# Performance work log

Hardware: AMD Instinct MI355X
Metric: run time of the kernel (lower is better)

The kernel has to match this reference:

```python
import jax, jax.numpy as jnp
import numpy as np

DIM = 1024
NUM_HEADS = 32
HEAD_DIM = 32
T = 2048
SCALE = 0.12
ROT_BASE = HEAD_DIM * 4  # Rotary(head_dim, max_seq_len, head_dim*4)
RMS_EPS = 1.1920929e-07  # torch float32 finfo eps (F.rms_norm default)


def _rms_norm(x):
    ms = jnp.mean(jnp.square(x), axis=-1, keepdims=True)
    return x * jax.lax.rsqrt(ms + RMS_EPS)


def _rotary_tables(seq_len):
    # modded-nanogpt half-truncated rotary: frequencies on first quarter, zeros on second
    quarter = HEAD_DIM // 4
    af = (1.0 / ROT_BASE) ** jnp.linspace(0.0, 1.0, quarter, dtype=jnp.float32)
    af = jnp.concatenate([af, jnp.zeros(quarter, dtype=jnp.float32)])  # [hd/2]
    theta = jnp.arange(seq_len, dtype=jnp.float32)[:, None] * af[None, :]  # [T, hd/2]
    return jnp.cos(theta), jnp.sin(theta)


def _apply_rotary(x, cos, sin):
    # x: [B, T, H, hd]; cos/sin: [T, hd/2]
    x1, x2 = jnp.split(x, 2, axis=-1)
    c = cos[None, :, None, :]
    s = sin[None, :, None, :]
    y1 = x1 * c + x2 * s
    y2 = -x1 * s + x2 * c
    return jnp.concatenate([y1, y2], axis=-1)


def setup_inputs() -> dict:
    key = jax.random.key(0)
    k1, k2, k3, k4 = jax.random.split(key, 4)
    std = 0.5 * DIM ** (-0.5)
    bound = (3.0 ** 0.5) * std
    x = jax.random.normal(k1, (1, T, DIM), dtype=jnp.float32)
    ve = jax.random.normal(k2, (1, T, NUM_HEADS * HEAD_DIM), dtype=jnp.float32)
    qkv_w = jax.random.uniform(k3, (3, NUM_HEADS * HEAD_DIM, DIM), dtype=jnp.float32,
                               minval=-bound, maxval=bound)
    lambdas = jnp.array([0.5, 0.5], dtype=jnp.float32)
    # original zero-inits c_proj; use small random so output/grads are nontrivial
    c_proj_w = jax.random.normal(k4, (DIM, NUM_HEADS * HEAD_DIM), dtype=jnp.float32) * 0.02
    return {"x": x, "ve": ve, "qkv_w": qkv_w, "lambdas": lambdas, "c_proj_w": c_proj_w}


def reference(x, ve, qkv_w, lambdas, c_proj_w):
    B, T_, D = x.shape
    H, hd = NUM_HEADS, HEAD_DIM
    # fused QKV projection: F.linear(x, qkv_w.flatten(end_dim=1))
    w = qkv_w.reshape(3 * H * hd, D)
    qkv = jnp.einsum('btd,ed->bte', x, w).reshape(B, T_, 3 * H, hd)
    q, k, v = jnp.split(qkv, 3, axis=2)  # each [B, T, H, hd]
    q = _rms_norm(q)
    k = _rms_norm(k)
    cos, sin = _rotary_tables(T_)
    q = _apply_rotary(q, cos, sin)
    k = _apply_rotary(k, cos, sin)
    v = lambdas[0] * v + lambdas[1] * ve.reshape(B, T_, H, hd)
    # causal attention with fixed scale 0.12
    scores = jnp.einsum('bqhd,bkhd->bhqk', q, k) * SCALE
    causal = jnp.tril(jnp.ones((T_, T_), dtype=bool))
    scores = jnp.where(causal[None, None, :, :], scores, -jnp.inf)
    attn = jax.nn.softmax(scores, axis=-1)
    y = jnp.einsum('bhqk,bkhd->bqhd', attn, v).reshape(B, T_, H * hd)
    return jnp.einsum('bte,de->btd', y, c_proj_w)
```

## Files before the change

kernel.cpp:

```cpp
#include <hip/hip_runtime.h>
#include <hip/hip_bf16.h>

#define NHEADS 32
#define HD_ 32
#define TSEQ 2048
#define SCALE_ 0.12f
#define LOG2E_ 1.44269504088896f
#define RMS_EPS_ 1.1920929e-07f

typedef unsigned short ushort_t;
typedef __bf16 bf16_t;
typedef __attribute__((ext_vector_type(8))) bf16_t bf16x8;
typedef __attribute__((ext_vector_type(4))) float f32x4;
typedef __attribute__((ext_vector_type(8))) unsigned short u16x8;

__device__ __forceinline__ ushort_t f2bfn(float f){
    __hip_bfloat16 b = __float2bfloat16(f);
    return *reinterpret_cast<ushort_t*>(&b);
}
__device__ __forceinline__ float bf2f(ushort_t s){
    union { unsigned u; float f; } v; v.u = ((unsigned)s) << 16;
    return v.f;
}
__device__ __forceinline__ float fexp2(float x){
#if __has_builtin(__builtin_amdgcn_exp2f)
    return __builtin_amdgcn_exp2f(x);
#else
    return exp2f(x);
#endif
}
__device__ __forceinline__ void gld16(const void* g, void* l){
    __builtin_amdgcn_global_load_lds(
        (const __attribute__((address_space(1))) unsigned int*)g,
        (__attribute__((address_space(3))) unsigned int*)l,
        16, 0, 0);
}

__global__ __launch_bounds__(256) void k_prep(const float* __restrict__ x,
                                              const float* __restrict__ qkw,
                                              const float* __restrict__ cpw,
                                              ushort_t* __restrict__ xb,
                                              ushort_t* __restrict__ wb,
                                              ushort_t* __restrict__ cpb,
                                              float* __restrict__ cost,
                                              float* __restrict__ sint)
{
    const int n1 = TSEQ * 1024 / 4, n2 = 3 * 1024 * 1024 / 4, n3 = 1024 * 1024 / 4;
    int i = blockIdx.x * 256 + threadIdx.x;
    if (i < n1 + n2 + n3){
        const float* src; ushort_t* dst; int j = i;
        if (j < n1){ src = x; dst = xb; }
        else if (j < n1 + n2){ j -= n1; src = qkw; dst = wb; }
        else { j -= n1 + n2; src = cpw; dst = cpb; }
        float4 v = ((const float4*)src)[j];
        ushort4 o;
        o.x = f2bfn(v.x); o.y = f2bfn(v.y); o.z = f2bfn(v.z); o.w = f2bfn(v.w);
        ((ushort4*)dst)[j] = o;
    } else {
        int g = i - (n1 + n2 + n3);
        if (g < TSEQ * 16){
            int t = g >> 4, ii = g & 15;
            float c = 1.0f, s = 0.0f;
            if (ii < 8){
                float af = powf(1.0f / 128.0f, (float)ii * (1.0f / 7.0f));
                sincosf((float)t * af, &s, &c);
            }
            cost[g] = c; sint[g] = s;
        }
    }
}

__global__ __launch_bounds__(256, 3) void k_gemm_qkv(const ushort_t* __restrict__ A,
                                                     const ushort_t* __restrict__ B,
                                                     const float* __restrict__ ve,
                                                     const float* __restrict__ lam,
                                                     const float* __restrict__ cost,
                                                     const float* __restrict__ sint,
                                                     ushort_t* __restrict__ qb,
                                                     ushort_t* __restrict__ kbuf,
                                                     ushort_t* __restrict__ vtb)
{
    const int K = 1024;
    __shared__ __align__(16) ushort_t As[2][128 * 32];
    __shared__ __align__(16) ushort_t Bs[2][64 * 32];
    const int tid = threadIdx.x;
    const int lane = tid & 63;
    const int w = tid >> 6;
    const int wr = w >> 1, wc = w & 1;
    const int l15 = lane & 15, hi = lane >> 4;
    const int m0 = blockIdx.y * 128, n0 = blockIdx.x * 64;
    const int sec = n0 >> 10;
    const int h = ((n0 & 1023) >> 5) + wc;
    const int srow = lane >> 2, scol = (lane & 3) * 8;

    f32x4 acc[4][2] = {};

    auto stage = [&](int k0, int buf){
        #pragma unroll
        for (int i = 0; i < 2; ++i){
            int c = w + i * 4;
            gld16(&A[(size_t)(m0 + c * 16 + srow) * K + k0 + scol], &As[buf][c * 512]);
        }
        gld16(&B[(size_t)(n0 + w * 16 + srow) * K + k0 + scol], &Bs[buf][w * 512]);
    };

    stage(0, 0);
    int cur = 0;
    for (int k0 = 0; k0 < K; k0 += 32){
        __syncthreads();
        if (k0 + 32 < K) stage(k0 + 32, cur ^ 1);
        bf16x8 af[4], bfr[2];
        #pragma unroll
        for (int mi = 0; mi < 4; ++mi)
            af[mi] = *(const bf16x8*)&As[cur][(wr * 64 + mi * 16 + l15) * 32 + hi * 8];
        #pragma unroll
        for (int ni = 0; ni < 2; ++ni)
            bfr[ni] = *(const bf16x8*)&Bs[cur][(wc * 32 + ni * 16 + l15) * 32 + hi * 8];
        #pragma unroll
        for (int mi = 0; mi < 4; ++mi)
            #pragma unroll
            for (int ni = 0; ni < 2; ++ni)
                acc[mi][ni] = __builtin_amdgcn_mfma_f32_16x16x32_bf16(af[mi], bfr[ni], acc[mi][ni], 0, 0, 0);
        cur ^= 1;
    }

    if (sec < 2){
        ushort_t* dst = (sec == 0) ? qb : kbuf;
        const float qscl = (sec == 0) ? SCALE_ * LOG2E_ : 1.0f;
        #pragma unroll
        for (int mi = 0; mi < 4; ++mi){
            #pragma unroll
            for (int r = 0; r < 4; ++r){
                const int t = m0 + wr * 64 + mi * 16 + hi * 4 + r;
                float v0 = acc[mi][0][r], v1 = acc[mi][1][r];
                float ss = v0 * v0 + v1 * v1;
                ss += __shfl_xor(ss, 1);
                ss += __shfl_xor(ss, 2);
                ss += __shfl_xor(ss, 4);
                ss += __shfl_xor(ss, 8);
                const float inv = rsqrtf(ss * (1.0f / 32.0f) + RMS_EPS_);
                const float c = cost[t * 16 + l15], s = sint[t * 16 + l15];
                const float n0v = v0 * inv, n1v = v1 * inv;
                const float o0 = (n0v * c + n1v * s) * qscl;
                const float o1 = (n1v * c - n0v * s) * qscl;
                size_t base = ((size_t)h * TSEQ + t) * 32;
                dst[base + l15]      = f2bfn(o0);
                dst[base + 16 + l15] = f2bfn(o1);
            }
        }
    } else {
        const float l0 = lam[0], l1 = lam[1];
        __syncthreads();
        ushort_t* vt = &As[0][0] + w * 2048;
        #pragma unroll
        for (int ni = 0; ni < 2; ++ni){
            const int d = ni * 16 + l15;
            #pragma unroll
            for (int mi = 0; mi < 4; ++mi){
                #pragma unroll
                for (int r = 0; r < 4; ++r){
                    const int t = m0 + wr * 64 + mi * 16 + hi * 4 + r;
                    const int tl = mi * 16 + hi * 4 + r;
                    float vef = ve[(size_t)t * 1024 + h * 32 + d];
                    float ov = l0 * acc[mi][ni][r] + l1 * vef;
                    const int g = (tl >> 3) ^ (d & 7);
                    vt[d * 64 + g * 8 + (tl & 7)] = f2bfn(ov);
                }
            }
        }
        __syncthreads();
        const int tc = lane & 7;
        #pragma unroll
        for (int p = 0; p < 4; ++p){
            const int d = p * 8 + (lane >> 3);
            const int g = tc ^ (d & 7);
            u16x8 o = *(const u16x8*)&vt[d * 64 + g * 8];
            *(u16x8*)&vtb[((size_t)h * HD_ + d) * TSEQ + m0 + wr * 64 + tc * 8] = o;
        }
    }
}

__global__ __launch_bounds__(256) void k_gemm_out(const ushort_t* __restrict__ A,
                                                  const ushort_t* __restrict__ B,
                                                  float* __restrict__ C,
                                                  int M, int N, int K)
{
    __shared__ __align__(16) ushort_t As[2][64 * 64];
    __shared__ __align__(16) ushort_t Bs[2][64 * 64];
    const int tid = threadIdx.x;
    const int lane = tid & 63;
    const int w = tid >> 6;
    const int wr = w >> 1, wc = w & 1;
    const int l15 = lane & 15, hi = lane >> 4;
    const int m0 = blockIdx.y * 64, n0 = blockIdx.x * 64;
    const int srow = lane >> 3, scol = (lane & 7) * 8;

    f32x4 acc[2][2] = {};

    auto stage = [&](int k0, int buf){
        #pragma unroll
        for (int i = 0; i < 2; ++i){
            int c = w * 2 + i;
            gld16(&A[(size_t)(m0 + c * 8 + srow) * K + k0 + scol], &As[buf][c * 512]);
            gld16(&B[(size_t)(n0 + c * 8 + srow) * K + k0 + scol], &Bs[buf][c * 512]);
        }
    };

    stage(0, 0);
    int cur = 0;
    for (int k0 = 0; k0 < K; k0 += 64){
        __syncthreads();
        if (k0 + 64 < K) stage(k0 + 64, cur ^ 1);
        bf16x8 af[2][2], bfr[2][2];
        #pragma unroll
        for (int mi = 0; mi < 2; ++mi)
            #pragma unroll
            for (int sub = 0; sub < 2; ++sub)
                af[mi][sub] = *(const bf16x8*)&As[cur][(wr * 32 + mi * 16 + l15) * 64 + sub * 32 + hi * 8];
        #pragma unroll
        for (int ni = 0; ni < 2; ++ni)
            #pragma unroll
            for (int sub = 0; sub < 2; ++sub)
                bfr[ni][sub] = *(const bf16x8*)&Bs[cur][(wc * 32 + ni * 16 + l15) * 64 + sub * 32 + hi * 8];
        #pragma unroll
        for (int sub = 0; sub < 2; ++sub)
            #pragma unroll
            for (int mi = 0; mi < 2; ++mi)
                #pragma unroll
                for (int ni = 0; ni < 2; ++ni)
                    acc[mi][ni] = __builtin_amdgcn_mfma_f32_16x16x32_bf16(af[mi][sub], bfr[ni][sub], acc[mi][ni], 0, 0, 0);
        cur ^= 1;
    }

    #pragma unroll
    for (int mi = 0; mi < 2; ++mi)
        #pragma unroll
        for (int ni = 0; ni < 2; ++ni)
            #pragma unroll
            for (int r = 0; r < 4; ++r){
                int row = m0 + wr * 32 + mi * 16 + hi * 4 + r;
                int col = n0 + wc * 32 + ni * 16 + l15;
                C[(size_t)row * N + col] = acc[mi][ni][r];
            }
}

template<bool MASK>
__device__ __forceinline__ void chain_step(const bf16x8* kf, const bf16x8* vv0, const bf16x8* vv1,
                                           ushort_t* pb, const bf16x8& qf,
                                           int kb0, int qrow, int l15, int hi,
                                           f32x4& a0, f32x4& a1, float& lp)
{
    f32x4 s[4];
    __builtin_amdgcn_s_setprio(1);
    #pragma unroll
    for (int ni = 0; ni < 4; ++ni){
        f32x4 z = {0.f, 0.f, 0.f, 0.f};
        s[ni] = __builtin_amdgcn_mfma_f32_16x16x32_bf16(kf[ni], qf, z, 0, 0, 0);
    }
    __builtin_amdgcn_s_setprio(0);
    if (MASK){
        const int relc = qrow - kb0 - 4 * hi;
        #pragma unroll
        for (int ni = 0; ni < 4; ++ni)
            #pragma unroll
            for (int r = 0; r < 4; ++r)
                if (16 * ni + r > relc) s[ni][r] = -1e30f;
    }
    float ps = 0.f;
    #pragma unroll
    for (int ni = 0; ni < 4; ++ni)
        #pragma unroll
        for (int r = 0; r < 4; ++r){
            float p = fexp2(s[ni][r]);
            s[ni][r] = p;
            ps += p;
        }
    lp += ps;
    #pragma unroll
    for (int ni = 0; ni < 4; ++ni){
        ushort4 pk;
        pk.x = f2bfn(s[ni][0]); pk.y = f2bfn(s[ni][1]);
        pk.z = f2bfn(s[ni][2]); pk.w = f2bfn(s[ni][3]);
        *(ushort4*)&pb[l15 * 72 + ni * 16 + hi * 4] = pk;
    }
    __builtin_amdgcn_s_setprio(1);
    #pragma unroll
    for (int kk = 0; kk < 2; ++kk){
        bf16x8 pf = *(const bf16x8*)&pb[l15 * 72 + kk * 32 + hi * 8];
        a0 = __builtin_amdgcn_mfma_f32_16x16x32_bf16(vv0[kk], pf, a0, 0, 0, 0);
        a1 = __builtin_amdgcn_mfma_f32_16x16x32_bf16(vv1[kk], pf, a1, 0, 0, 0);
    }
    __builtin_amdgcn_s_setprio(0);
}

__global__ __launch_bounds__(256, 4) void k_attn(const ushort_t* __restrict__ qb,
                                                 const ushort_t* __restrict__ kb,
                                                 const ushort_t* __restrict__ vtb,
                                                 ushort_t* __restrict__ yb)
{
    const int bid = blockIdx.x;
    const int xcd = bid & 7, idx = bid >> 3;
    const int h  = xcd * 4 + (idx & 3);
    const int qt = 31 - (idx >> 2);
    const int tid = threadIdx.x;
    const int w = tid >> 6, lane = tid & 63;
    const int l15 = lane & 15, hi = lane >> 4;

    __shared__ __align__(16) ushort_t Kbuf[2][64 * 32];
    __shared__ __align__(16) ushort_t Vbuf[2][32 * 64];
    __shared__ __align__(16) ushort_t Pbuf[4][16 * 72];

    const ushort_t* kb_h = kb + (size_t)h * TSEQ * HD_;
    const ushort_t* vt_h = vtb + (size_t)h * HD_ * TSEQ;
    const ushort_t* qb_h = qb + (size_t)h * TSEQ * HD_;

    const int qw = qt * 64 + w * 16;
    const bf16x8 qf = *(const bf16x8*)&qb_h[(size_t)(qw + l15) * 32 + hi * 8];

    const int krow = w * 16 + (lane >> 2);
    const int kcol = (lane & 3) * 8;
    const int vrow = w * 8 + (lane >> 3);
    const int vslot = (lane & 7) ^ (vrow & 7);
    auto stage = [&](int kt, int buf){
        const int kb0 = kt * 64;
        gld16(&kb_h[(size_t)(kb0 + krow) * 32 + kcol], &Kbuf[buf][w * 512]);
        gld16(&vt_h[(size_t)vrow * TSEQ + kb0 + vslot * 8], &Vbuf[buf][w * 512]);
    };

    f32x4 a0 = {0.f,0.f,0.f,0.f}, a1 = a0;
    float lp = 0.f;
    ushort_t* pb = &Pbuf[w][0];

    const int nT = qt + 1;
    stage(0, 0);
    int cur = 0;
    for (int kt = 0; kt < nT; ++kt){
        __syncthreads();
        if (kt + 1 < nT) stage(kt + 1, cur ^ 1);
        const int kb0 = kt * 64;
        bf16x8 kf[4], vv0[2], vv1[2];
        #pragma unroll
        for (int ni = 0; ni < 4; ++ni)
            kf[ni] = *(const bf16x8*)&Kbuf[cur][(ni * 16 + l15) * 32 + hi * 8];
        #pragma unroll
        for (int kk = 0; kk < 2; ++kk){
            int sl = kk * 4 + hi;
            vv0[kk] = *(const bf16x8*)&Vbuf[cur][l15 * 64 + (sl ^ (l15 & 7)) * 8];
            vv1[kk] = *(const bf16x8*)&Vbuf[cur][(16 + l15) * 64 + (sl ^ (l15 & 7)) * 8];
        }
        if (kt < qt)
            chain_step<false>(kf, vv0, vv1, pb, qf, kb0, qw + l15, l15, hi, a0, a1, lp);
        else
            chain_step<true >(kf, vv0, vv1, pb, qf, kb0, qw + l15, l15, hi, a0, a1, lp);
        cur ^= 1;
    }

    lp += __shfl_xor(lp, 16);
    lp += __shfl_xor(lp, 32);
    float inv = 1.0f / lp;
    ushort4 o0, o1;
    o0.x = f2bfn(a0[0]*inv); o0.y = f2bfn(a0[1]*inv);
    o0.z = f2bfn(a0[2]*inv); o0.w = f2bfn(a0[3]*inv);
    o1.x = f2bfn(a1[0]*inv); o1.y = f2bfn(a1[1]*inv);
    o1.z = f2bfn(a1[2]*inv); o1.w = f2bfn(a1[3]*inv);
    size_t base = (size_t)(qw + l15) * 1024 + h * 32;
    *(ushort4*)&yb[base + hi * 4]      = o0;
    *(ushort4*)&yb[base + 16 + hi * 4] = o1;
}

extern "C" void kernel_launch(void* const* d_in, const int* in_sizes, int n_in,
                              void* d_out, int out_size, void* d_ws, size_t ws_size,
                              hipStream_t stream)
{
    const float* x   = (const float*)d_in[0];
    const float* ve  = (const float*)d_in[1];
    const float* qkw = (const float*)d_in[2];
    const float* lam = (const float*)d_in[3];
    const float* cpw = (const float*)d_in[4];

    char* ws = (char*)d_ws;
    size_t o = 0;
    auto take = [&](size_t bytes) -> char* {
        char* p = ws + o; o += (bytes + 255) & ~(size_t)255; return p;
    };
    ushort_t* xb   = (ushort_t*)take((size_t)TSEQ * 1024 * 2);
    ushort_t* wb   = (ushort_t*)take((size_t)3072 * 1024 * 2);
    ushort_t* cpb  = (ushort_t*)take((size_t)1024 * 1024 * 2);
    float*    cost = (float*)take((size_t)TSEQ * 16 * 4);
    float*    sint = (float*)take((size_t)TSEQ * 16 * 4);
    ushort_t* qb   = (ushort_t*)take((size_t)NHEADS * TSEQ * HD_ * 2);
    ushort_t* kb   = (ushort_t*)take((size_t)NHEADS * TSEQ * HD_ * 2 + 8192);
    ushort_t* vtb  = (ushort_t*)take((size_t)NHEADS * HD_ * TSEQ * 2 + 8192);
    ushort_t* yb   = xb;

    const int prep_items = (TSEQ * 1024 + 3 * 1024 * 1024 + 1024 * 1024) / 4 + TSEQ * 16;
    k_prep<<<(prep_items + 255) / 256, 256, 0, stream>>>(x, qkw, cpw, xb, wb, cpb, cost, sint);
    k_gemm_qkv<<<dim3(48, 16), 256, 0, stream>>>(xb, wb, ve, lam, cost, sint, qb, kb, vtb);
    k_attn<<<1024, 256, 0, stream>>>(qb, kb, vtb, yb);
    k_gemm_out<<<dim3(1024 / 64, TSEQ / 64), 256, 0, stream>>>(yb, cpb, (float*)d_out, TSEQ, 1024, 1024);
}
```

Measured before the change: 152.0 us.

## Fuse fp32-to-bf16 conversion and rotary tables into GEMMs, drop prep kernel

The separate prep kernel that cast x, qkv_w and c_proj_w to bf16 and precomputed cos/sin tables is removed. The QKV and output GEMMs now load fp32 tiles into registers, convert them to bf16 and write them to swizzled LDS, and rotary sin/cos is computed inline. Block indices are remapped with an XCD-aware grid. The attention K tile also gets an XOR swizzle against LDS bank conflicts. This saves one launch plus a full pass writing and rereading the bf16 copies. In exchange, the GEMMs read twice the global bytes per element and do conversion work on the critical path, because global_load_lds is replaced by register staging.

```diff
diff --git a/kernel.cpp b/kernel.cpp
--- a/kernel.cpp
+++ b/kernel.cpp
@@ -18,10 +18,6 @@
     __hip_bfloat16 b = __float2bfloat16(f);
     return *reinterpret_cast<ushort_t*>(&b);
 }
-__device__ __forceinline__ float bf2f(ushort_t s){
-    union { unsigned u; float f; } v; v.u = ((unsigned)s) << 16;
-    return v.f;
-}
 __device__ __forceinline__ float fexp2(float x){
 #if __has_builtin(__builtin_amdgcn_exp2f)
     return __builtin_amdgcn_exp2f(x);
@@ -35,47 +31,17 @@
         (__attribute__((address_space(3))) unsigned int*)l,
         16, 0, 0);
 }
-
-__global__ __launch_bounds__(256) void k_prep(const float* __restrict__ x,
-                                              const float* __restrict__ qkw,
-                                              const float* __restrict__ cpw,
-                                              ushort_t* __restrict__ xb,
-                                              ushort_t* __restrict__ wb,
-                                              ushort_t* __restrict__ cpb,
-                                              float* __restrict__ cost,
-                                              float* __restrict__ sint)
-{
-    const int n1 = TSEQ * 1024 / 4, n2 = 3 * 1024 * 1024 / 4, n3 = 1024 * 1024 / 4;
-    int i = blockIdx.x * 256 + threadIdx.x;
-    if (i < n1 + n2 + n3){
-        const float* src; ushort_t* dst; int j = i;
-        if (j < n1){ src = x; dst = xb; }
-        else if (j < n1 + n2){ j -= n1; src = qkw; dst = wb; }
-        else { j -= n1 + n2; src = cpw; dst = cpb; }
-        float4 v = ((const float4*)src)[j];
-        ushort4 o;
-        o.x = f2bfn(v.x); o.y = f2bfn(v.y); o.z = f2bfn(v.z); o.w = f2bfn(v.w);
-        ((ushort4*)dst)[j] = o;
-    } else {
-        int g = i - (n1 + n2 + n3);
-        if (g < TSEQ * 16){
-            int t = g >> 4, ii = g & 15;
-            float c = 1.0f, s = 0.0f;
-            if (ii < 8){
-                float af = powf(1.0f / 128.0f, (float)ii * (1.0f / 7.0f));
-                sincosf((float)t * af, &s, &c);
-            }
-            cost[g] = c; sint[g] = s;
-        }
-    }
-}
-
-__global__ __launch_bounds__(256, 3) void k_gemm_qkv(const ushort_t* __restrict__ A,
-                                                     const ushort_t* __restrict__ B,
+__device__ __forceinline__ u16x8 pack8(float4 a, float4 b){
+    u16x8 o;
+    o[0]=f2bfn(a.x); o[1]=f2bfn(a.y); o[2]=f2bfn(a.z); o[3]=f2bfn(a.w);
+    o[4]=f2bfn(b.x); o[5]=f2bfn(b.y); o[6]=f2bfn(b.z); o[7]=f2bfn(b.w);
+    return o;
+}
+
+__global__ __launch_bounds__(256, 3) void k_gemm_qkv(const float* __restrict__ X,
+                                                     const float* __restrict__ W,
                                                      const float* __restrict__ ve,
                                                      const float* __restrict__ lam,
-                                                     const float* __restrict__ cost,
-                                                     const float* __restrict__ sint,
                                                      ushort_t* __restrict__ qb,
                                                      ushort_t* __restrict__ kbuf,
                                                      ushort_t* __restrict__ vtb)
@@ -88,34 +54,50 @@
     const int w = tid >> 6;
     const int wr = w >> 1, wc = w & 1;
     const int l15 = lane & 15, hi = lane >> 4;
-    const int m0 = blockIdx.y * 128, n0 = blockIdx.x * 64;
-    const int sec = n0 >> 10;
-    const int h = ((n0 & 1023) >> 5) + wc;
-    const int srow = lane >> 2, scol = (lane & 3) * 8;
+
+    const int bid = blockIdx.x;
+    const int xcd = bid & 7, j = bid >> 3;
+    const int m0 = (xcd * 2 + (j & 1)) * 128;
+    const int nidx = j >> 1;
+    const int n0 = nidx * 64;
+    const int sec = nidx >> 4;
+    const int h = ((nidx & 15) << 1) + wc;
+
+    const int arow = tid >> 1, ahalf = tid & 1;
+    const int brow = tid >> 2, bq = tid & 3;
+    const int akey = (arow >> 1) & 3;
+    const int bkey = (brow >> 1) & 3;
+    float4 ra[4], rb[2];
+
+    auto loadRegs = [&](int k0){
+        const float4* pa = (const float4*)&X[(size_t)(m0 + arow) * K + k0 + ahalf * 16];
+        ra[0] = pa[0]; ra[1] = pa[1]; ra[2] = pa[2]; ra[3] = pa[3];
+        const float4* pb = (const float4*)&W[(size_t)(n0 + brow) * K + k0 + bq * 8];
+        rb[0] = pb[0]; rb[1] = pb[1];
+    };
+    auto writeLDS = [&](int buf){
+        *(u16x8*)&As[buf][arow * 32 + ((ahalf * 2 + 0) ^ akey) * 8] = pack8(ra[0], ra[1]);
+        *(u16x8*)&As[buf][arow * 32 + ((ahalf * 2 + 1) ^ akey) * 8] = pack8(ra[2], ra[3]);
+        *(u16x8*)&Bs[buf][brow * 32 + (bq ^ bkey) * 8] = pack8(rb[0], rb[1]);
+    };
 
     f32x4 acc[4][2] = {};
-
-    auto stage = [&](int k0, int buf){
-        #pragma unroll
-        for (int i = 0; i < 2; ++i){
-            int c = w + i * 4;
-            gld16(&A[(size_t)(m0 + c * 16 + srow) * K + k0 + scol], &As[buf][c * 512]);
-        }
-        gld16(&B[(size_t)(n0 + w * 16 + srow) * K + k0 + scol], &Bs[buf][w * 512]);
-    };
-
-    stage(0, 0);
+    const int kq = (l15 >> 1) & 3;
+    const int soff = (hi ^ kq) * 8;
+
+    loadRegs(0);
     int cur = 0;
     for (int k0 = 0; k0 < K; k0 += 32){
-        __syncthreads();
-        if (k0 + 32 < K) stage(k0 + 32, cur ^ 1);
+        writeLDS(cur);
+        __syncthreads();
+        if (k0 + 32 < K) loadRegs(k0 + 32);
         bf16x8 af[4], bfr[2];
         #pragma unroll
         for (int mi = 0; mi < 4; ++mi)
-            af[mi] = *(const bf16x8*)&As[cur][(wr * 64 + mi * 16 + l15) * 32 + hi * 8];
+            af[mi] = *(const bf16x8*)&As[cur][(wr * 64 + mi * 16 + l15) * 32 + soff];
         #pragma unroll
         for (int ni = 0; ni < 2; ++ni)
-            bfr[ni] = *(const bf16x8*)&Bs[cur][(wc * 32 + ni * 16 + l15) * 32 + hi * 8];
+            bfr[ni] = *(const bf16x8*)&Bs[cur][(wc * 32 + ni * 16 + l15) * 32 + soff];
         #pragma unroll
         for (int mi = 0; mi < 4; ++mi)
             #pragma unroll
@@ -127,6 +109,7 @@
     if (sec < 2){
         ushort_t* dst = (sec == 0) ? qb : kbuf;
         const float qscl = (sec == 0) ? SCALE_ * LOG2E_ : 1.0f;
+        const float fs = exp2f(-(float)l15);
         #pragma unroll
         for (int mi = 0; mi < 4; ++mi){
             #pragma unroll
@@ -139,7 +122,8 @@
                 ss += __shfl_xor(ss, 4);
                 ss += __shfl_xor(ss, 8);
                 const float inv = rsqrtf(ss * (1.0f / 32.0f) + RMS_EPS_);
-                const float c = cost[t * 16 + l15], s = sint[t * 16 + l15];
+                float c = 1.0f, s = 0.0f;
+                if (l15 < 8) sincosf((float)t * fs, &s, &c);
                 const float n0v = v0 * inv, n1v = v1 * inv;
                 const float o0 = (n0v * c + n1v * s) * qscl;
                 const float o1 = (n1v * c - n0v * s) * qscl;
@@ -180,48 +164,67 @@
     }
 }
 
-__global__ __launch_bounds__(256) void k_gemm_out(const ushort_t* __restrict__ A,
-                                                  const ushort_t* __restrict__ B,
-                                                  float* __restrict__ C,
-                                                  int M, int N, int K)
-{
-    __shared__ __align__(16) ushort_t As[2][64 * 64];
-    __shared__ __align__(16) ushort_t Bs[2][64 * 64];
+__global__ __launch_bounds__(256, 3) void k_gemm_out(const ushort_t* __restrict__ A,
+                                                     const float* __restrict__ W2,
+                                                     float* __restrict__ C)
+{
+    const int K = 1024, N = 1024;
+    __shared__ __align__(16) ushort_t As2[2][64 * 64];
+    __shared__ __align__(16) ushort_t Bs2[2][64 * 64];
     const int tid = threadIdx.x;
     const int lane = tid & 63;
     const int w = tid >> 6;
     const int wr = w >> 1, wc = w & 1;
     const int l15 = lane & 15, hi = lane >> 4;
-    const int m0 = blockIdx.y * 64, n0 = blockIdx.x * 64;
-    const int srow = lane >> 3, scol = (lane & 7) * 8;
-
-    f32x4 acc[2][2] = {};
-
-    auto stage = [&](int k0, int buf){
+
+    const int bid = blockIdx.x;
+    const int xcd = bid & 7, j = bid >> 3;
+    const int m0 = (xcd * 4 + (j & 3)) * 64;
+    const int n0 = (j >> 2) * 64;
+
+    const int srow = lane >> 3;
+    const int sslot = (lane & 7) ^ srow;
+    const int brow = tid >> 2, bq = tid & 3;
+    const int bkey = brow & 7;
+    float4 rb[4];
+
+    auto stageA = [&](int k0, int buf){
         #pragma unroll
         for (int i = 0; i < 2; ++i){
             int c = w * 2 + i;
-            gld16(&A[(size_t)(m0 + c * 8 + srow) * K + k0 + scol], &As[buf][c * 512]);
-            gld16(&B[(size_t)(n0 + c * 8 + srow) * K + k0 + scol], &Bs[buf][c * 512]);
-        }
-    };
-
-    stage(0, 0);
+            gld16(&A[(size_t)(m0 + c * 8 + srow) * K + k0 + sslot * 8], &As2[buf][c * 512]);
+        }
+    };
+    auto loadB = [&](int k0){
+        const float4* p = (const float4*)&W2[(size_t)(n0 + brow) * K + k0 + bq * 16];
+        rb[0] = p[0]; rb[1] = p[1]; rb[2] = p[2]; rb[3] = p[3];
+    };
+    auto writeB = [&](int buf){
+        *(u16x8*)&Bs2[buf][brow * 64 + ((bq * 2 + 0) ^ bkey) * 8] = pack8(rb[0], rb[1]);
+        *(u16x8*)&Bs2[buf][brow * 64 + ((bq * 2 + 1) ^ bkey) * 8] = pack8(rb[2], rb[3]);
+    };
+
+    f32x4 acc[2][2] = {};
+    const int rkey = l15 & 7;
+
+    loadB(0);
+    stageA(0, 0);
     int cur = 0;
     for (int k0 = 0; k0 < K; k0 += 64){
-        __syncthreads();
-        if (k0 + 64 < K) stage(k0 + 64, cur ^ 1);
+        writeB(cur);
+        __syncthreads();
+        if (k0 + 64 < K){ stageA(k0 + 64, cur ^ 1); loadB(k0 + 64); }
         bf16x8 af[2][2], bfr[2][2];
         #pragma unroll
         for (int mi = 0; mi < 2; ++mi)
             #pragma unroll
             for (int sub = 0; sub < 2; ++sub)
-                af[mi][sub] = *(const bf16x8*)&As[cur][(wr * 32 + mi * 16 + l15) * 64 + sub * 32 + hi * 8];
+                af[mi][sub] = *(const bf16x8*)&As2[cur][(wr * 32 + mi * 16 + l15) * 64 + ((sub * 4 + hi) ^ rkey) * 8];
         #pragma unroll
         for (int ni = 0; ni < 2; ++ni)
             #pragma unroll
             for (int sub = 0; sub < 2; ++sub)
-                bfr[ni][sub] = *(const bf16x8*)&Bs[cur][(wc * 32 + ni * 16 + l15) * 64 + sub * 32 + hi * 8];
+                bfr[ni][sub] = *(const bf16x8*)&Bs2[cur][(wc * 32 + ni * 16 + l15) * 64 + ((sub * 4 + hi) ^ rkey) * 8];
         #pragma unroll
         for (int sub = 0; sub < 2; ++sub)
             #pragma unroll
@@ -318,18 +321,19 @@
     const bf16x8 qf = *(const bf16x8*)&qb_h[(size_t)(qw + l15) * 32 + hi * 8];
 
     const int krow = w * 16 + (lane >> 2);
-    const int kcol = (lane & 3) * 8;
+    const int kslot = (lane & 3) ^ ((lane >> 3) & 3);
     const int vrow = w * 8 + (lane >> 3);
     const int vslot = (lane & 7) ^ (vrow & 7);
     auto stage = [&](int kt, int buf){
         const int kb0 = kt * 64;
-        gld16(&kb_h[(size_t)(kb0 + krow) * 32 + kcol], &Kbuf[buf][w * 512]);
+        gld16(&kb_h[(size_t)(kb0 + krow) * 32 + kslot * 8], &Kbuf[buf][w * 512]);
         gld16(&vt_h[(size_t)vrow * TSEQ + kb0 + vslot * 8], &Vbuf[buf][w * 512]);
     };
 
     f32x4 a0 = {0.f,0.f,0.f,0.f}, a1 = a0;
     float lp = 0.f;
     ushort_t* pb = &Pbuf[w][0];
+    const int kq = (l15 >> 1) & 3;
 
     const int nT = qt + 1;
     stage(0, 0);
@@ -341,7 +345,7 @@
         bf16x8 kf[4], vv0[2], vv1[2];
         #pragma unroll
         for (int ni = 0; ni < 4; ++ni)
-            kf[ni] = *(const bf16x8*)&Kbuf[cur][(ni * 16 + l15) * 32 + hi * 8];
+            kf[ni] = *(const bf16x8*)&Kbuf[cur][(ni * 16 + l15) * 32 + (hi ^ kq) * 8];
         #pragma unroll
         for (int kk = 0; kk < 2; ++kk){
             int sl = kk * 4 + hi;
@@ -383,19 +387,12 @@
     auto take = [&](size_t bytes) -> char* {
         char* p = ws + o; o += (bytes + 255) & ~(size_t)255; return p;
     };
-    ushort_t* xb   = (ushort_t*)take((size_t)TSEQ * 1024 * 2);
-    ushort_t* wb   = (ushort_t*)take((size_t)3072 * 1024 * 2);
-    ushort_t* cpb  = (ushort_t*)take((size_t)1024 * 1024 * 2);
-    float*    cost = (float*)take((size_t)TSEQ * 16 * 4);
-    float*    sint = (float*)take((size_t)TSEQ * 16 * 4);
-    ushort_t* qb   = (ushort_t*)take((size_t)NHEADS * TSEQ * HD_ * 2);
-    ushort_t* kb   = (ushort_t*)take((size_t)NHEADS * TSEQ * HD_ * 2 + 8192);
-    ushort_t* vtb  = (ushort_t*)take((size_t)NHEADS * HD_ * TSEQ * 2 + 8192);
-    ushort_t* yb   = xb;
-
-    const int prep_items = (TSEQ * 1024 + 3 * 1024 * 1024 + 1024 * 1024) / 4 + TSEQ * 16;
-    k_prep<<<(prep_items + 255) / 256, 256, 0, stream>>>(x, qkw, cpw, xb, wb, cpb, cost, sint);
-    k_gemm_qkv<<<dim3(48, 16), 256, 0, stream>>>(xb, wb, ve, lam, cost, sint, qb, kb, vtb);
+    ushort_t* qb  = (ushort_t*)take((size_t)NHEADS * TSEQ * HD_ * 2);
+    ushort_t* kb  = (ushort_t*)take((size_t)NHEADS * TSEQ * HD_ * 2);
+    ushort_t* vtb = (ushort_t*)take((size_t)NHEADS * HD_ * TSEQ * 2);
+    ushort_t* yb  = (ushort_t*)take((size_t)TSEQ * 1024 * 2);
+
+    k_gemm_qkv<<<768, 256, 0, stream>>>(x, qkw, ve, lam, qb, kb, vtb);
     k_attn<<<1024, 256, 0, stream>>>(qb, kb, vtb, yb);
-    k_gemm_out<<<dim3(1024 / 64, TSEQ / 64), 256, 0, stream>>>(yb, cpb, (float*)d_out, TSEQ, 1024, 1024);
-}
+    k_gemm_out<<<512, 256, 0, stream>>>(yb, cpw, (float*)d_out);
+}
```

Result: slower. 162.2 us (+6.7%).
